# Performance work log

Measured on AMD Instinct MI355X. Metric: run time of the kernel, lower is better.

The kernel has to match this reference:

```python
import jax, jax.numpy as jnp
import numpy as np

B, F, L, D = 256, 4, 64, 768
HID = (F + F) * 200  # 1600
NEG = -1e10


def setup_inputs() -> dict:
    key = jax.random.key(0)
    ks = jax.random.split(key, 8)
    left = jax.random.normal(ks[0], (B, F, L, D), dtype=jnp.float32)
    right = jax.random.normal(ks[1], (B, F, L, D), dtype=jnp.float32)
    # emulate ragged padding: last quarter of tokens are zero (masked out)
    left = left.at[:, :, 3 * L // 4 :, :].set(0.0)
    right = right.at[:, :, 3 * L // 4 :, :].set(0.0)
    femb_l = jax.random.normal(ks[2], (F, D), dtype=jnp.float32)
    femb_r = jax.random.normal(ks[3], (F, D), dtype=jnp.float32)
    empty_attr = jax.random.normal(ks[4], (D,), dtype=jnp.float32) * 0.05
    in_dim = 2 * F * D
    W1 = jax.random.normal(ks[5], (HID, in_dim), dtype=jnp.float32) * (1.0 / np.sqrt(in_dim))
    b1 = jnp.zeros((HID,), dtype=jnp.float32)
    W2 = jax.random.normal(ks[6], (2, HID), dtype=jnp.float32) * (1.0 / np.sqrt(HID))
    b2 = jnp.full((2,), -np.log((1 - 0.01) / 0.01), dtype=jnp.float32)
    return {"left": left, "right": right, "femb_l": femb_l, "femb_r": femb_r,
            "empty_attr": empty_attr, "W1": W1, "b1": b1, "W2": W2, "b2": b2}


def _attribute_matching(v, femb, empty_attr):
    # v: [B, F, L, D], femb: [F, D]
    tok_mask = (v != 0).sum(axis=-1) > 0          # [B, F, L]
    attr_mask = tok_mask.any(axis=-1)              # [B, F]
    logits = jnp.einsum('bfld,fd->bfl', v, femb)   # per-field attention scores
    logits = logits + jnp.where(tok_mask, 0.0, NEG)
    w = jax.nn.softmax(logits, axis=2)             # masked softmax over tokens
    summary = jnp.einsum('bfl,bfld->bfd', w, v)    # attention pooling
    return jnp.where(attr_mask[..., None], summary, empty_attr)  # [B, F, D]


def reference(left, right, femb_l, femb_r, empty_attr, W1, b1, W2, b2):
    l_rep = _attribute_matching(left, femb_l, empty_attr)
    r_rep = _attribute_matching(right, femb_r, empty_attr)
    concat = jnp.concatenate([l_rep, r_rep], axis=1).reshape(left.shape[0], -1)
    h = jax.nn.relu(concat @ W1.T + b1)
    return h @ W2.T + b2  # [B, 2]
```

## Files before the change

kernel.cpp:

```cpp
#include <hip/hip_runtime.h>

typedef __attribute__((ext_vector_type(8))) short short8;
typedef __attribute__((ext_vector_type(4))) short short4_t;
typedef __attribute__((ext_vector_type(4))) float f32x4;

#define NEGBIG -1e10f

__device__ __forceinline__ unsigned short f2bf(float x) {
  unsigned int u = __float_as_uint(x);
  u += 0x7FFFu + ((u >> 16) & 1u);
  return (unsigned short)(u >> 16);
}

__device__ __forceinline__ float4 mul4(float4 a, float s) {
  float4 r; r.x = a.x*s; r.y = a.y*s; r.z = a.z*s; r.w = a.w*s; return r;
}
__device__ __forceinline__ float4 add4(float4 a, float4 b) {
  float4 r; r.x = a.x+b.x; r.y = a.y+b.y; r.z = a.z+b.z; r.w = a.w+b.w; return r;
}
__device__ __forceinline__ float4 upd4(float4 a, float sc, float e, float4 x) {
  float4 r;
  r.x = a.x*sc + e*x.x; r.y = a.y*sc + e*x.y;
  r.z = a.z*sc + e*x.z; r.w = a.w*sc + e*x.w;
  return r;
}

__global__ __launch_bounds__(256, 6) void pool_kernel(
    const float* __restrict__ left, const float* __restrict__ right,
    const float* __restrict__ femb_l, const float* __restrict__ femb_r,
    const float* __restrict__ empty_attr,
    unsigned short* __restrict__ concat)
{
  int bid  = blockIdx.x;
  int side = bid >> 10;
  int rem  = bid & 1023;
  int f    = rem & 3;
  int b    = rem >> 2;
  const float* v    = (side ? right : left) + (size_t)rem * 64 * 768;
  const float* femb = (side ? femb_r : femb_l) + f * 768;

  int tid = threadIdx.x, wave = tid >> 6, lane = tid & 63;

  const float4* fp = (const float4*)femb;
  float4 f0 = fp[lane], f1 = fp[lane + 64], f2 = fp[lane + 128];

  float4 a0 = {0,0,0,0}, a1 = {0,0,0,0}, a2 = {0,0,0,0};
  float m = -3.0e38f, s = 0.f;
  int wnz = 0;

  const float4* vp = (const float4*)(v + (size_t)wave * 16 * 768);
  #pragma unroll 2
  for (int t = 0; t < 16; ++t) {
    float4 x0 = vp[t * 192 + lane];
    float4 x1 = vp[t * 192 + 64 + lane];
    float4 x2 = vp[t * 192 + 128 + lane];

    float dot = x0.x*f0.x + x0.y*f0.y + x0.z*f0.z + x0.w*f0.w
              + x1.x*f1.x + x1.y*f1.y + x1.z*f1.z + x1.w*f1.w
              + x2.x*f2.x + x2.y*f2.y + x2.z*f2.z + x2.w*f2.w;
    int nz = (x0.x!=0.f) | (x0.y!=0.f) | (x0.z!=0.f) | (x0.w!=0.f)
           | (x1.x!=0.f) | (x1.y!=0.f) | (x1.z!=0.f) | (x1.w!=0.f)
           | (x2.x!=0.f) | (x2.y!=0.f) | (x2.z!=0.f) | (x2.w!=0.f);
    #pragma unroll
    for (int sh = 32; sh > 0; sh >>= 1) dot += __shfl_xor(dot, sh);
    int any_nz = __any(nz);
    wnz |= any_nz;
    float logit = any_nz ? dot : dot + NEGBIG;

    float mn = fmaxf(m, logit);
    float e  = __expf(logit - mn);
    float sc = __expf(m - mn);
    s  = s * sc + e;
    a0 = upd4(a0, sc, e, x0);
    a1 = upd4(a1, sc, e, x1);
    a2 = upd4(a2, sc, e, x2);
    m  = mn;
  }

  __shared__ float m_lds[4], s_lds[4];
  __shared__ int   nz_lds[4];
  __shared__ float acc_lds[4 * 768];

  if (lane == 0) { m_lds[wave] = m; nz_lds[wave] = wnz; }
  __syncthreads();
  float M = fmaxf(fmaxf(m_lds[0], m_lds[1]), fmaxf(m_lds[2], m_lds[3]));
  float scale = __expf(m - M);
  if (lane == 0) s_lds[wave] = s * scale;
  float4* al = (float4*)acc_lds;
  al[wave * 192 +       lane] = mul4(a0, scale);
  al[wave * 192 +  64 + lane] = mul4(a1, scale);
  al[wave * 192 + 128 + lane] = mul4(a2, scale);
  __syncthreads();

  if (tid < 192) {
    float4 A = add4(add4(al[tid], al[192 + tid]),
                    add4(al[384 + tid], al[576 + tid]));
    float S = s_lds[0] + s_lds[1] + s_lds[2] + s_lds[3];
    int has = nz_lds[0] | nz_lds[1] | nz_lds[2] | nz_lds[3];
    float4 r;
    if (has) { float inv = 1.f / S; r = mul4(A, inv); }
    else     { r = ((const float4*)empty_attr)[tid]; }
    ushort4 o;
    o.x = f2bf(r.x); o.y = f2bf(r.y); o.z = f2bf(r.z); o.w = f2bf(r.w);
    size_t base = ((size_t)b * 8 + side * 4 + f) * 192;
    ((ushort4*)concat)[base + tid] = o;
  }
}

__global__ __launch_bounds__(256) void gemm1_kernel(
    const unsigned short* __restrict__ A,
    const float* __restrict__ W1,
    float* __restrict__ Hpart)
{
  const int K = 6144, N = 1600, KC = 768;
  int colb = blockIdx.x;
  int kc   = blockIdx.y;
  int col0 = colb * 16;
  int tid = threadIdx.x, wave = tid >> 6, lane = tid & 63;

  __shared__ short wlds[96 * 16 * 8];

  const float* wsrc = W1 + (size_t)col0 * K + kc * KC;
  #pragma unroll
  for (int i = 0; i < 12; ++i) {
    int flat4 = tid + 256 * i;
    int col = flat4 / 192;
    int k   = (flat4 % 192) * 4;
    float4 w = *(const float4*)(wsrc + (size_t)col * K + k);
    short4_t o;
    o[0] = (short)f2bf(w.x); o[1] = (short)f2bf(w.y);
    o[2] = (short)f2bf(w.z); o[3] = (short)f2bf(w.w);
    *(short4_t*)(wlds + (k >> 3) * 128 + col * 8 + (k & 7)) = o;
  }
  __syncthreads();

  int lr = lane & 15, lk = (lane >> 4) * 8;
  const short* a0 = (const short*)A + (size_t)(wave * 64 + lr) * K + kc * KC + lk;
  const short* bptr = wlds + (lane >> 4) * 128 + lr * 8;

  f32x4 acc0 = {}, acc1 = {}, acc2 = {}, acc3 = {};

  #pragma unroll 4
  for (int ks = 0; ks < 24; ++ks) {
    short8 bf  = *(const short8*)(bptr + ks * 512);
    short8 af0 = *(const short8*)(a0 + ks * 32);
    short8 af1 = *(const short8*)(a0 + ks * 32 + 16 * K);
    short8 af2 = *(const short8*)(a0 + ks * 32 + 32 * K);
    short8 af3 = *(const short8*)(a0 + ks * 32 + 48 * K);
    acc0 = __builtin_amdgcn_mfma_f32_16x16x32_bf16(af0, bf, acc0, 0, 0, 0);
    acc1 = __builtin_amdgcn_mfma_f32_16x16x32_bf16(af1, bf, acc1, 0, 0, 0);
    acc2 = __builtin_amdgcn_mfma_f32_16x16x32_bf16(af2, bf, acc2, 0, 0, 0);
    acc3 = __builtin_amdgcn_mfma_f32_16x16x32_bf16(af3, bf, acc3, 0, 0, 0);
  }

  int ccol = lane & 15;
  int crow = (lane >> 4) * 4;
  float* hp = Hpart + (size_t)kc * 256 * N + (size_t)col0 + ccol;
  f32x4 accs[4] = {acc0, acc1, acc2, acc3};
  #pragma unroll
  for (int i = 0; i < 4; ++i) {
    int r = wave * 64 + i * 16 + crow;
    #pragma unroll
    for (int q = 0; q < 4; ++q)
      hp[(size_t)(r + q) * N] = accs[i][q];
  }
}

__global__ __launch_bounds__(256) void epilogue_kernel(
    const float* __restrict__ Hpart, const float* __restrict__ b1,
    const float* __restrict__ W2, const float* __restrict__ b2,
    float* __restrict__ out)
{
  const int N = 1600;
  int b = blockIdx.x, tid = threadIdx.x;
  int wave = tid >> 6, lane = tid & 63;
  float s0 = 0.f, s1 = 0.f;
  for (int c = tid; c < N; c += 256) {
    float acc = 0.f;
    #pragma unroll
    for (int kc = 0; kc < 8; ++kc)
      acc += Hpart[((size_t)kc * 256 + b) * N + c];
    float h = fmaxf(acc + b1[c], 0.f);
    s0 += h * W2[c];
    s1 += h * W2[N + c];
  }
  #pragma unroll
  for (int s = 32; s > 0; s >>= 1) {
    s0 += __shfl_xor(s0, s);
    s1 += __shfl_xor(s1, s);
  }
  __shared__ float r0[4], r1[4];
  if (lane == 0) { r0[wave] = s0; r1[wave] = s1; }
  __syncthreads();
  if (tid == 0) {
    out[b * 2 + 0] = r0[0] + r0[1] + r0[2] + r0[3] + b2[0];
    out[b * 2 + 1] = r1[0] + r1[1] + r1[2] + r1[3] + b2[1];
  }
}

extern "C" void kernel_launch(void* const* d_in, const int* in_sizes, int n_in,
                              void* d_out, int out_size, void* d_ws, size_t ws_size,
                              hipStream_t stream) {
  const float* left       = (const float*)d_in[0];
  const float* right      = (const float*)d_in[1];
  const float* femb_l     = (const float*)d_in[2];
  const float* femb_r     = (const float*)d_in[3];
  const float* empty_attr = (const float*)d_in[4];
  const float* W1         = (const float*)d_in[5];
  const float* b1         = (const float*)d_in[6];
  const float* W2         = (const float*)d_in[7];
  const float* b2         = (const float*)d_in[8];
  float* out = (float*)d_out;

  char* ws = (char*)d_ws;
  unsigned short* concat = (unsigned short*)ws;
  float*          Hpart  = (float*)(ws + 3145728);

  hipLaunchKernelGGL(pool_kernel, dim3(2048), dim3(256), 0, stream,
                     left, right, femb_l, femb_r, empty_attr, concat);
  hipLaunchKernelGGL(gemm1_kernel, dim3(100, 8), dim3(256), 0, stream,
                     concat, W1, Hpart);
  hipLaunchKernelGGL(epilogue_kernel, dim3(256), dim3(256), 0, stream,
                     Hpart, b1, W2, b2, out);
}
```

Measured before the change: 137.1 us.

## Restructure pooling into 8-wave two-pass softmax with bf16-packed token cache

```diff
diff --git a/kernel.cpp b/kernel.cpp
--- a/kernel.cpp
+++ b/kernel.cpp
@@ -11,6 +11,14 @@
   u += 0x7FFFu + ((u >> 16) & 1u);
   return (unsigned short)(u >> 16);
 }
+__device__ __forceinline__ unsigned pack2(float a, float b) {
+  unsigned ua = __float_as_uint(a), ub = __float_as_uint(b);
+  ua += 0x7FFFu + ((ua >> 16) & 1u);
+  ub += 0x7FFFu + ((ub >> 16) & 1u);
+  return (ua >> 16) | (ub & 0xFFFF0000u);
+}
+__device__ __forceinline__ float lo_bf(unsigned p) { return __uint_as_float(p << 16); }
+__device__ __forceinline__ float hi_bf(unsigned p) { return __uint_as_float(p & 0xFFFF0000u); }
 
 __device__ __forceinline__ float4 mul4(float4 a, float s) {
   float4 r; r.x = a.x*s; r.y = a.y*s; r.z = a.z*s; r.w = a.w*s; return r;
@@ -18,14 +26,8 @@
 __device__ __forceinline__ float4 add4(float4 a, float4 b) {
   float4 r; r.x = a.x+b.x; r.y = a.y+b.y; r.z = a.z+b.z; r.w = a.w+b.w; return r;
 }
-__device__ __forceinline__ float4 upd4(float4 a, float sc, float e, float4 x) {
-  float4 r;
-  r.x = a.x*sc + e*x.x; r.y = a.y*sc + e*x.y;
-  r.z = a.z*sc + e*x.z; r.w = a.w*sc + e*x.w;
-  return r;
-}
-
-__global__ __launch_bounds__(256, 6) void pool_kernel(
+
+__global__ __launch_bounds__(512, 3) void pool_kernel(
     const float* __restrict__ left, const float* __restrict__ right,
     const float* __restrict__ femb_l, const float* __restrict__ femb_r,
     const float* __restrict__ empty_attr,
@@ -44,62 +46,99 @@
   const float4* fp = (const float4*)femb;
   float4 f0 = fp[lane], f1 = fp[lane + 64], f2 = fp[lane + 128];
 
-  float4 a0 = {0,0,0,0}, a1 = {0,0,0,0}, a2 = {0,0,0,0};
-  float m = -3.0e38f, s = 0.f;
-  int wnz = 0;
-
-  const float4* vp = (const float4*)(v + (size_t)wave * 16 * 768);
-  #pragma unroll 2
-  for (int t = 0; t < 16; ++t) {
+  const float4* vp = (const float4*)(v + (size_t)wave * 8 * 768);
+
+  float d[8];
+  unsigned pk0[8], pk1[8], pk2[8], pk3[8], pk4[8], pk5[8];
+  unsigned nzmask = 0;
+
+  #pragma unroll
+  for (int t = 0; t < 8; ++t) {
     float4 x0 = vp[t * 192 + lane];
     float4 x1 = vp[t * 192 + 64 + lane];
     float4 x2 = vp[t * 192 + 128 + lane];
-
-    float dot = x0.x*f0.x + x0.y*f0.y + x0.z*f0.z + x0.w*f0.w
-              + x1.x*f1.x + x1.y*f1.y + x1.z*f1.z + x1.w*f1.w
-              + x2.x*f2.x + x2.y*f2.y + x2.z*f2.z + x2.w*f2.w;
-    int nz = (x0.x!=0.f) | (x0.y!=0.f) | (x0.z!=0.f) | (x0.w!=0.f)
-           | (x1.x!=0.f) | (x1.y!=0.f) | (x1.z!=0.f) | (x1.w!=0.f)
-           | (x2.x!=0.f) | (x2.y!=0.f) | (x2.z!=0.f) | (x2.w!=0.f);
-    #pragma unroll
-    for (int sh = 32; sh > 0; sh >>= 1) dot += __shfl_xor(dot, sh);
-    int any_nz = __any(nz);
-    wnz |= any_nz;
-    float logit = any_nz ? dot : dot + NEGBIG;
-
-    float mn = fmaxf(m, logit);
-    float e  = __expf(logit - mn);
-    float sc = __expf(m - mn);
-    s  = s * sc + e;
-    a0 = upd4(a0, sc, e, x0);
-    a1 = upd4(a1, sc, e, x1);
-    a2 = upd4(a2, sc, e, x2);
-    m  = mn;
-  }
-
-  __shared__ float m_lds[4], s_lds[4];
-  __shared__ int   nz_lds[4];
-  __shared__ float acc_lds[4 * 768];
-
-  if (lane == 0) { m_lds[wave] = m; nz_lds[wave] = wnz; }
-  __syncthreads();
-  float M = fmaxf(fmaxf(m_lds[0], m_lds[1]), fmaxf(m_lds[2], m_lds[3]));
-  float scale = __expf(m - M);
-  if (lane == 0) s_lds[wave] = s * scale;
+    d[t] = x0.x*f0.x + x0.y*f0.y + x0.z*f0.z + x0.w*f0.w
+         + x1.x*f1.x + x1.y*f1.y + x1.z*f1.z + x1.w*f1.w
+         + x2.x*f2.x + x2.y*f2.y + x2.z*f2.z + x2.w*f2.w;
+    unsigned nzb = __float_as_uint(x0.x) | __float_as_uint(x0.y)
+                 | __float_as_uint(x0.z) | __float_as_uint(x0.w)
+                 | __float_as_uint(x1.x) | __float_as_uint(x1.y)
+                 | __float_as_uint(x1.z) | __float_as_uint(x1.w)
+                 | __float_as_uint(x2.x) | __float_as_uint(x2.y)
+                 | __float_as_uint(x2.z) | __float_as_uint(x2.w);
+    nzmask |= (nzb != 0u) ? (1u << t) : 0u;
+    pk0[t] = pack2(x0.x, x0.y); pk1[t] = pack2(x0.z, x0.w);
+    pk2[t] = pack2(x1.x, x1.y); pk3[t] = pack2(x1.z, x1.w);
+    pk4[t] = pack2(x2.x, x2.y); pk5[t] = pack2(x2.z, x2.w);
+  }
+
+  #pragma unroll
+  for (int sh = 32; sh > 0; sh >>= 1) {
+    d[0] += __shfl_xor(d[0], sh);
+    d[1] += __shfl_xor(d[1], sh);
+    d[2] += __shfl_xor(d[2], sh);
+    d[3] += __shfl_xor(d[3], sh);
+    d[4] += __shfl_xor(d[4], sh);
+    d[5] += __shfl_xor(d[5], sh);
+    d[6] += __shfl_xor(d[6], sh);
+    d[7] += __shfl_xor(d[7], sh);
+    nzmask |= __shfl_xor(nzmask, sh);
+  }
+
+  float l[8], e[8];
+  #pragma unroll
+  for (int t = 0; t < 8; ++t)
+    l[t] = d[t] + (((nzmask >> t) & 1u) ? 0.f : NEGBIG);
+  float m01 = fmaxf(l[0], l[1]), m23 = fmaxf(l[2], l[3]);
+  float m45 = fmaxf(l[4], l[5]), m67 = fmaxf(l[6], l[7]);
+  float m_w = fmaxf(fmaxf(m01, m23), fmaxf(m45, m67));
+  #pragma unroll
+  for (int t = 0; t < 8; ++t) e[t] = __expf(l[t] - m_w);
+  float s_w = ((e[0]+e[1]) + (e[2]+e[3])) + ((e[4]+e[5]) + (e[6]+e[7]));
+
+  __shared__ float m_lds[8], s_lds[8];
+  __shared__ int   nz_lds[8];
+  __shared__ float acc_lds[8 * 768];
+
+  if (lane == 0) { m_lds[wave] = m_w; s_lds[wave] = s_w; nz_lds[wave] = (nzmask != 0u); }
+
+  float4 A0 = {0,0,0,0}, A1 = {0,0,0,0}, A2 = {0,0,0,0};
+  #pragma unroll
+  for (int t = 0; t < 8; ++t) {
+    float c = e[t];
+    A0.x += c * lo_bf(pk0[t]); A0.y += c * hi_bf(pk0[t]);
+    A0.z += c * lo_bf(pk1[t]); A0.w += c * hi_bf(pk1[t]);
+    A1.x += c * lo_bf(pk2[t]); A1.y += c * hi_bf(pk2[t]);
+    A1.z += c * lo_bf(pk3[t]); A1.w += c * hi_bf(pk3[t]);
+    A2.x += c * lo_bf(pk4[t]); A2.y += c * hi_bf(pk4[t]);
+    A2.z += c * lo_bf(pk5[t]); A2.w += c * hi_bf(pk5[t]);
+  }
+
+  __syncthreads();
+  float M = m_lds[0];
+  #pragma unroll
+  for (int w = 1; w < 8; ++w) M = fmaxf(M, m_lds[w]);
+  float S = 0.f;
+  #pragma unroll
+  for (int w = 0; w < 8; ++w) S += s_lds[w] * __expf(m_lds[w] - M);
+  float scale = __expf(m_w - M) / S;
+
   float4* al = (float4*)acc_lds;
-  al[wave * 192 +       lane] = mul4(a0, scale);
-  al[wave * 192 +  64 + lane] = mul4(a1, scale);
-  al[wave * 192 + 128 + lane] = mul4(a2, scale);
+  al[wave * 192 +       lane] = mul4(A0, scale);
+  al[wave * 192 +  64 + lane] = mul4(A1, scale);
+  al[wave * 192 + 128 + lane] = mul4(A2, scale);
   __syncthreads();
 
   if (tid < 192) {
-    float4 A = add4(add4(al[tid], al[192 + tid]),
-                    add4(al[384 + tid], al[576 + tid]));
-    float S = s_lds[0] + s_lds[1] + s_lds[2] + s_lds[3];
-    int has = nz_lds[0] | nz_lds[1] | nz_lds[2] | nz_lds[3];
+    float4 A = add4(add4(add4(al[tid], al[192 + tid]),
+                         add4(al[384 + tid], al[576 + tid])),
+                    add4(add4(al[768 + tid], al[960 + tid]),
+                         add4(al[1152 + tid], al[1344 + tid])));
+    int has = nz_lds[0] | nz_lds[1] | nz_lds[2] | nz_lds[3]
+            | nz_lds[4] | nz_lds[5] | nz_lds[6] | nz_lds[7];
     float4 r;
-    if (has) { float inv = 1.f / S; r = mul4(A, inv); }
-    else     { r = ((const float4*)empty_attr)[tid]; }
+    if (has) r = A;
+    else     r = ((const float4*)empty_attr)[tid];
     ushort4 o;
     o.x = f2bf(r.x); o.y = f2bf(r.y); o.z = f2bf(r.z); o.w = f2bf(r.w);
     size_t base = ((size_t)b * 8 + side * 4 + f) * 192;
@@ -134,8 +173,8 @@
   }
   __syncthreads();
 
-  int lr = lane & 15, lk = (lane >> 4) * 8;
-  const short* a0 = (const short*)A + (size_t)(wave * 64 + lr) * K + kc * KC + lk;
+  int lr = lane & 15;
+  const short* a0 = (const short*)A + (size_t)(wave * 64 + lr) * K + kc * KC + (lane >> 4) * 8;
   const short* bptr = wlds + (lane >> 4) * 128 + lr * 8;
 
   f32x4 acc0 = {}, acc1 = {}, acc2 = {}, acc3 = {};
@@ -216,7 +255,7 @@
   unsigned short* concat = (unsigned short*)ws;
   float*          Hpart  = (float*)(ws + 3145728);
 
-  hipLaunchKernelGGL(pool_kernel, dim3(2048), dim3(256), 0, stream,
+  hipLaunchKernelGGL(pool_kernel, dim3(2048), dim3(512), 0, stream,
                      left, right, femb_l, femb_r, empty_attr, concat);
   hipLaunchKernelGGL(gemm1_kernel, dim3(100, 8), dim3(256), 0, stream,
                      concat, W1, Hpart);
```

Measured after the change: 144.3 us. 1.05x slower.
